# Kernel tuning notes

Measured on AMD Instinct MI355X. Metric: run time of the kernel, lower is better.

Reference implementation:

```python
import jax, jax.numpy as jnp
import numpy as np

N, E, G, C, H, O = 100000, 600000, 1000, 2, 128, 10
HC = H // 2  # cls MLP hidden

def _bn(x, g, b, rm, rv):
    # eval-mode BatchNorm1d with running stats
    return (x - rm) * jax.lax.rsqrt(rv + 1e-5) * g + b

def setup_inputs() -> dict:
    key = jax.random.key(0)
    ks = iter(jax.random.split(key, 64))
    rn = lambda shape, s=0.05: jax.random.normal(next(ks), shape, jnp.float32) * s
    inp = {
        'pos': jax.random.normal(next(ks), (N, C), jnp.float32),
        'edge_index': jax.random.randint(next(ks), (2, E), 0, N),
        'batch': jnp.sort(jax.random.randint(next(ks), (N,), 0, G)),
    }
    def bn_params(pfx):
        return {pfx+'g': jnp.ones((H,), jnp.float32), pfx+'b': jnp.zeros((H,), jnp.float32),
                pfx+'rm': rn((H,)), pfx+'rv': jax.random.uniform(next(ks), (H,), jnp.float32, 0.5, 1.5)}
    # conv1 nn: Lin(C,H)-ReLU-Lin(H,H)-ReLU-BN
    inp.update(W1a=rn((C, H)), b1a=jnp.zeros((H,)), W1b=rn((H, H)), b1b=jnp.zeros((H,)))
    inp.update(bn_params('n1_'))
    # conv2 nn: Lin(H,H)-ReLU-Lin(H,H)-ReLU-BN
    inp.update(W2a=rn((H, H)), b2a=jnp.zeros((H,)), W2b=rn((H, H)), b2b=jnp.zeros((H,)))
    inp.update(bn_params('n2_'))
    # fc1: Lin(C,H)-ReLU-BN ; fc2: Lin(H,H)-ReLU-BN (weights SHARED for both fc2 calls)
    inp.update(Wf1=rn((C, H)), bf1=jnp.zeros((H,)))
    inp.update(bn_params('f1_'))
    inp.update(Wf2=rn((H, H)), bf2=jnp.zeros((H,)))
    inp.update(bn_params('f2_'))
    # cls MLP: Lin(H,HC)-BN-PReLU-Lin(HC,O)
    inp.update(Wc1=rn((H, HC)), bc1=jnp.zeros((HC,)),
               gc=jnp.ones((HC,), jnp.float32), bec=jnp.zeros((HC,), jnp.float32),
               rmc=rn((HC,)), rvc=jax.random.uniform(next(ks), (HC,), jnp.float32, 0.5, 1.5),
               a_prelu=jnp.asarray(0.25, jnp.float32),
               Wc2=rn((HC, O)), bc2=jnp.zeros((O,)))
    return inp


def reference(pos, edge_index, batch,
              W1a, b1a, W1b, b1b, n1_g, n1_b, n1_rm, n1_rv,
              W2a, b2a, W2b, b2b, n2_g, n2_b, n2_rm, n2_rv,
              Wf1, bf1, f1_g, f1_b, f1_rm, f1_rv,
              Wf2, bf2, f2_g, f2_b, f2_rm, f2_rv,
              Wc1, bc1, gc, bec, rmc, rvc, a_prelu, Wc2, bc2):
    src, dst = edge_index[0], edge_index[1]

    def gin_nn(h, Wa, ba, Wb, bb, g, b, rm, rv):
        h = jax.nn.relu(h @ Wa + ba)
        h = jax.nn.relu(h @ Wb + bb)
        return _bn(h, g, b, rm, rv)

    def gin(x, Wa, ba, Wb, bb, g, b, rm, rv):
        # GINConv, eps=0: nn((1+eps)*x + sum_{j in N(i)} x_j)
        agg = jax.ops.segment_sum(x[src], dst, num_segments=N)
        return gin_nn(x + agg, Wa, ba, Wb, bb, g, b, rm, rv)

    def fc(x, W, b, g, be, rm, rv):
        return _bn(jax.nn.relu(x @ W + b), g, be, rm, rv)

    pool = lambda h: jax.ops.segment_sum(h, batch, num_segments=G)

    x0_g = fc(pool(pos), Wf1, bf1, f1_g, f1_b, f1_rm, f1_rv)           # [G,H]
    x1 = gin(pos, W1a, b1a, W1b, b1b, n1_g, n1_b, n1_rm, n1_rv)        # [N,H]
    x1_g = fc(x0_g + pool(x1), Wf2, bf2, f2_g, f2_b, f2_rm, f2_rv)     # [G,H]
    x2 = gin(x1, W2a, b2a, W2b, b2b, n2_g, n2_b, n2_rm, n2_rv)         # [N,H]
    x2_g = fc(x0_g + x1_g + pool(x2), Wf2, bf2, f2_g, f2_b, f2_rm, f2_rv)

    # dropout inactive in eval; cls MLP with PReLU
    h = x2_g @ Wc1 + bc1
    h = _bn(h, gc, bec, rmc, rvc)
    h = jnp.where(h > 0, h, a_prelu * h)
    return h @ Wc2 + bc2  # [G,O]
```

## Files before the change

kernel.cpp:

```cpp
#include <hip/hip_runtime.h>

#define H 128
#define HC 64
#define NOUT 10

static constexpr int kN = 100000;
static constexpr int kE = 600000;
static constexpr int kG = 1000;

typedef __attribute__((ext_vector_type(8))) short short8v;
typedef __attribute__((ext_vector_type(4))) float f32x4;

__device__ __forceinline__ float4 ld4(const float* p) { return *(const float4*)p; }

__device__ __forceinline__ unsigned f2bf(float f) {
    unsigned u = __float_as_uint(f);
    return (u + 0x7fffu + ((u >> 16) & 1u)) >> 16;
}
__device__ __forceinline__ unsigned f2bf2(float a, float b) {
    return f2bf(a) | (f2bf(b) << 16);
}
__device__ __forceinline__ void unpack_add8(uint4 u, float* a) {
    a[0] += __uint_as_float(u.x << 16); a[1] += __uint_as_float(u.x & 0xFFFF0000u);
    a[2] += __uint_as_float(u.y << 16); a[3] += __uint_as_float(u.y & 0xFFFF0000u);
    a[4] += __uint_as_float(u.z << 16); a[5] += __uint_as_float(u.z & 0xFFFF0000u);
    a[6] += __uint_as_float(u.w << 16); a[7] += __uint_as_float(u.w & 0xFFFF0000u);
}

__device__ __forceinline__ int swzmask(int rl) { return (rl & 15) << 3; }

__global__ void k_setup(int* __restrict__ deg,
                        const float* __restrict__ Wa, const float* __restrict__ Wb,
                        const float* __restrict__ Wc, unsigned short* __restrict__ wpk,
                        const int* __restrict__ batch, int* __restrict__ browptr,
                        const float* __restrict__ Wf2, float* __restrict__ Wf2T,
                        const float* __restrict__ Wc1, float* __restrict__ Wc1T) {
    int gt = blockIdx.x * blockDim.x + threadIdx.x;
    if (gt < 25000) {
        ((int4*)deg)[gt] = make_int4(0, 0, 0, 0);
    } else if (gt < 31144) {
        int gt2 = gt - 25000;
        int m = gt2 >> 11, t = gt2 & 2047;
        const float* W = (m == 0) ? Wa : (m == 1) ? Wb : Wc;
        int lane = t & 63, fc = t >> 6;
        int kb = fc >> 3, c16 = fc & 7;
        int col = c16 * 16 + (lane & 15);
        int k0 = kb * 32 + (lane >> 4) * 8;
        unsigned r[4];
#pragma unroll
        for (int p = 0; p < 4; ++p) {
            float a = W[(size_t)(k0 + 2 * p) * H + col];
            float b = W[(size_t)(k0 + 2 * p + 1) * H + col];
            r[p] = f2bf2(a, b);
        }
        *(uint4*)(wpk + (size_t)m * 16384 + (size_t)t * 8) = make_uint4(r[0], r[1], r[2], r[3]);
    } else if (gt < 32145) {
        int g = gt - 31144;
        int lo = 0, hi = kN;
        while (lo < hi) {
            int mid = (lo + hi) >> 1;
            if (batch[mid] < g) lo = mid + 1; else hi = mid;
        }
        browptr[g] = lo;
    } else if (gt < 36241) {
        int id = gt - 32145;
        int col = id >> 5, j4 = id & 31;
        float4 v;
        v.x = Wf2[(j4 * 4 + 0) * H + col];
        v.y = Wf2[(j4 * 4 + 1) * H + col];
        v.z = Wf2[(j4 * 4 + 2) * H + col];
        v.w = Wf2[(j4 * 4 + 3) * H + col];
        ((float4*)Wf2T)[col * 32 + j4] = v;
    } else if (gt < 38289) {
        int id = gt - 36241;
        int t64 = id >> 5, j4 = id & 31;
        float4 v;
        v.x = Wc1[(j4 * 4 + 0) * HC + t64];
        v.y = Wc1[(j4 * 4 + 1) * HC + t64];
        v.z = Wc1[(j4 * 4 + 2) * HC + t64];
        v.w = Wc1[(j4 * 4 + 3) * HC + t64];
        ((float4*)Wc1T)[t64 * 32 + j4] = v;
    }
}

__global__ void k_hist(const int* __restrict__ keys, int* __restrict__ cnt, int n) {
    int i = blockIdx.x * blockDim.x + threadIdx.x;
    if (i < n) atomicAdd(&cnt[keys[i]], 1);
}

__global__ void k_scan_p1(const int* __restrict__ in, int* __restrict__ partial, int n) {
    __shared__ int red[256];
    int b = blockIdx.x, t = threadIdx.x;
    int base = b * 1024 + t * 4;
    int s = 0;
#pragma unroll
    for (int k = 0; k < 4; ++k) {
        int j = base + k;
        if (j < n) s += in[j];
    }
    red[t] = s;
    __syncthreads();
    for (int off = 128; off; off >>= 1) {
        if (t < off) red[t] += red[t + off];
        __syncthreads();
    }
    if (t == 0) partial[b] = red[0];
}

__global__ void k_scan_p3(const int* __restrict__ in, const int* __restrict__ partial,
                          int* __restrict__ out, int* __restrict__ cursor, int n, int nb) {
    __shared__ int bb[256];
    __shared__ int red[256];
    int b = blockIdx.x, t = threadIdx.x;
    bb[t] = (t < b) ? partial[t] : 0;
    __syncthreads();
    for (int off = 128; off; off >>= 1) {
        if (t < off) bb[t] += bb[t + off];
        __syncthreads();
    }
    int bbase = bb[0];

    int base = b * 1024 + t * 4;
    int v[4];
    int s = 0;
#pragma unroll
    for (int k = 0; k < 4; ++k) {
        int j = base + k;
        v[k] = (j < n) ? in[j] : 0;
        s += v[k];
    }
    red[t] = s;
    __syncthreads();
    for (int off = 1; off < 256; off <<= 1) {
        int u = (t >= off) ? red[t - off] : 0;
        __syncthreads();
        red[t] += u;
        __syncthreads();
    }
    int tbase = bbase + red[t] - s;
#pragma unroll
    for (int k = 0; k < 4; ++k) {
        int j = base + k;
        if (j < n) {
            out[j] = tbase;
            if (cursor) cursor[j] = tbase;
            tbase += v[k];
        }
    }
    if (b == nb - 1 && t == 255) out[n] = bbase + red[255];
}

__global__ void k_scatter(const int* __restrict__ src, const int* __restrict__ dst,
                          int* __restrict__ cursor, int* __restrict__ eidx, int E) {
    int e = blockIdx.x * blockDim.x + threadIdx.x;
    if (e >= E) return;
    int slot = atomicAdd(&cursor[dst[e]], 1);
    eidx[slot] = src[e];
}

__global__ void k_gather_add(const int* __restrict__ rowptr, const int* __restrict__ eidx,
                             const unsigned short* __restrict__ x, unsigned short* __restrict__ out,
                             int nN) {
    int idx = blockIdx.x * blockDim.x + threadIdx.x;
    int i = idx >> 4, q = idx & 15;
    if (i >= nN) return;
    const int off = q * 8;
    float a[8] = {0, 0, 0, 0, 0, 0, 0, 0};
    unpack_add8(*(const uint4*)(x + (size_t)i * H + off), a);
    int j0 = rowptr[i], j1 = rowptr[i + 1];
    int j = j0;
    for (; j + 4 <= j1; j += 4) {
        int e0 = eidx[j], e1 = eidx[j + 1], e2 = eidx[j + 2], e3 = eidx[j + 3];
        uint4 u0 = *(const uint4*)(x + (size_t)e0 * H + off);
        uint4 u1 = *(const uint4*)(x + (size_t)e1 * H + off);
        uint4 u2 = *(const uint4*)(x + (size_t)e2 * H + off);
        uint4 u3 = *(const uint4*)(x + (size_t)e3 * H + off);
        unpack_add8(u0, a); unpack_add8(u1, a);
        unpack_add8(u2, a); unpack_add8(u3, a);
    }
    for (; j < j1; ++j) {
        int s = eidx[j];
        unpack_add8(*(const uint4*)(x + (size_t)s * H + off), a);
    }
    *(uint4*)(out + (size_t)i * H + off) =
        make_uint4(f2bf2(a[0], a[1]), f2bf2(a[2], a[3]), f2bf2(a[4], a[5]), f2bf2(a[6], a[7]));
}

__global__ __launch_bounds__(256) void k_gin1(
    const float* __restrict__ pos,
    const int* __restrict__ rowptr, const int* __restrict__ eidx,
    const float* __restrict__ W1a, const float* __restrict__ b1a,
    const short8v* __restrict__ wpk, const float* __restrict__ bias,
    const float* __restrict__ bn_g, const float* __restrict__ bn_b,
    const float* __restrict__ bn_rm, const float* __restrict__ bn_rv,
    unsigned short* __restrict__ out, int nN) {
    __shared__ unsigned short As[H * H];
    __shared__ float sB[H], sS[H], sH2[H];
    const int t = threadIdx.x;

    if (t < H) {
        sB[t] = bias[t];
        float s = bn_g[t] * rsqrtf(bn_rv[t] + 1e-5f);
        sS[t] = s;
        sH2[t] = bn_b[t] - bn_rm[t] * s;
    }

    {
        const int rl = t >> 1, half = t & 1;
        const int ic = min(blockIdx.x * 128 + rl, nN - 1);
        float2 p = ((const float2*)pos)[ic];
        float x0 = half ? 0.f : p.x;
        float x1 = half ? 0.f : p.y;
        int j0 = rowptr[ic], j1 = rowptr[ic + 1];
        int j = j0 + half;
        for (; j + 2 < j1; j += 4) {
            int e0 = eidx[j], e1 = eidx[j + 2];
            float2 q0 = ((const float2*)pos)[e0];
            float2 q1 = ((const float2*)pos)[e1];
            x0 += q0.x + q1.x; x1 += q0.y + q1.y;
        }
        for (; j < j1; j += 2) {
            float2 q = ((const float2*)pos)[eidx[j]];
            x0 += q.x; x1 += q.y;
        }
        x0 += __shfl_xor(x0, 1);
        x1 += __shfl_xor(x1, 1);

        const int mask = swzmask(rl);
#pragma unroll
        for (int c4 = 0; c4 < 16; ++c4) {
            int c = half * 64 + c4 * 4;
            float4 w0 = ld4(&W1a[c]);
            float4 w1 = ld4(&W1a[H + c]);
            float4 bb = ld4(&b1a[c]);
            float r0 = fmaxf(x0 * w0.x + x1 * w1.x + bb.x, 0.f);
            float r1 = fmaxf(x0 * w0.y + x1 * w1.y + bb.y, 0.f);
            float r2 = fmaxf(x0 * w0.z + x1 * w1.z + bb.z, 0.f);
            float r3 = fmaxf(x0 * w0.w + x1 * w1.w + bb.w, 0.f);
            int idx = rl * H + c;
            *(uint2*)(As + (idx ^ mask)) = make_uint2(f2bf2(r0, r1), f2bf2(r2, r3));
        }
    }
    __syncthreads();

    const int lane = t & 63;
    const int wave = t >> 6;
    const int rowbase = blockIdx.x * 128 + wave * 32;
    const int lrow = lane & 15;
    const int lhi = lane >> 4;

    f32x4 acc[2][8];
#pragma unroll
    for (int rr = 0; rr < 2; ++rr)
#pragma unroll
        for (int c = 0; c < 8; ++c) acc[rr][c] = (f32x4){0.f, 0.f, 0.f, 0.f};

#pragma unroll
    for (int kb = 0; kb < 4; ++kb) {
        short8v xf[2];
#pragma unroll
        for (int rr = 0; rr < 2; ++rr) {
            int rl = wave * 32 + rr * 16 + lrow;
            int idx = rl * H + kb * 32 + lhi * 8;
            xf[rr] = *(const short8v*)(As + (idx ^ swzmask(rl)));
        }
#pragma unroll
        for (int c16 = 0; c16 < 8; ++c16) {
            short8v wf = wpk[(kb * 8 + c16) * 64 + lane];
            acc[0][c16] = __builtin_amdgcn_mfma_f32_16x16x32_bf16(wf, xf[0], acc[0][c16], 0, 0, 0);
            acc[1][c16] = __builtin_amdgcn_mfma_f32_16x16x32_bf16(wf, xf[1], acc[1][c16], 0, 0, 0);
        }
    }

#pragma unroll
    for (int c16 = 0; c16 < 8; ++c16) {
        const int c0 = c16 * 16 + lhi * 4;
        float b0 = sB[c0], b1 = sB[c0 + 1], b2 = sB[c0 + 2], b3 = sB[c0 + 3];
        float s0 = sS[c0], s1 = sS[c0 + 1], s2 = sS[c0 + 2], s3 = sS[c0 + 3];
        float h0 = sH2[c0], h1 = sH2[c0 + 1], h2 = sH2[c0 + 2], h3 = sH2[c0 + 3];
#pragma unroll
        for (int rr = 0; rr < 2; ++rr) {
            int row = rowbase + rr * 16 + lrow;
            if (row >= nN) continue;
            float v0 = fmaxf(acc[rr][c16][0] + b0, 0.f) * s0 + h0;
            float v1 = fmaxf(acc[rr][c16][1] + b1, 0.f) * s1 + h1;
            float v2 = fmaxf(acc[rr][c16][2] + b2, 0.f) * s2 + h2;
            float v3 = fmaxf(acc[rr][c16][3] + b3, 0.f) * s3 + h3;
            *(uint2*)(out + (size_t)row * H + c0) = make_uint2(f2bf2(v0, v1), f2bf2(v2, v3));
        }
    }
}

__global__ __launch_bounds__(256) void k_gin2(
    const unsigned short* __restrict__ xin, const short8v* __restrict__ wpA,
    const float* __restrict__ biasA, const short8v* __restrict__ wpB,
    const float* __restrict__ biasB,
    const float* __restrict__ bn_g, const float* __restrict__ bn_b,
    const float* __restrict__ bn_rm, const float* __restrict__ bn_rv,
    unsigned short* __restrict__ out, int nN) {
    __shared__ unsigned short As[H * H];
    __shared__ float sBa[H], sBb[H], sS[H], sH2[H];
    const int t = threadIdx.x;

    if (t < H) {
        sBa[t] = biasA[t];
        sBb[t] = biasB[t];
        float s = bn_g[t] * rsqrtf(bn_rv[t] + 1e-5f);
        sS[t] = s;
        sH2[t] = bn_b[t] - bn_rm[t] * s;
    }
    __syncthreads();

    const int lane = t & 63;
    const int wave = t >> 6;
    const int rowbase = blockIdx.x * 128 + wave * 32;
    const int lrow = lane & 15;
    const int lhi = lane >> 4;

    f32x4 acc[2][8];
#pragma unroll
    for (int rr = 0; rr < 2; ++rr)
#pragma unroll
        for (int c = 0; c < 8; ++c) acc[rr][c] = (f32x4){0.f, 0.f, 0.f, 0.f};

#pragma unroll
    for (int kb = 0; kb < 4; ++kb) {
        short8v xf[2];
#pragma unroll
        for (int rr = 0; rr < 2; ++rr) {
            int row = rowbase + rr * 16 + lrow;
            row = row < nN ? row : nN - 1;
            xf[rr] = *(const short8v*)(xin + (size_t)row * H + kb * 32 + lhi * 8);
        }
#pragma unroll
        for (int c16 = 0; c16 < 8; ++c16) {
            short8v wf = wpA[(kb * 8 + c16) * 64 + lane];
            acc[0][c16] = __builtin_amdgcn_mfma_f32_16x16x32_bf16(wf, xf[0], acc[0][c16], 0, 0, 0);
            acc[1][c16] = __builtin_amdgcn_mfma_f32_16x16x32_bf16(wf, xf[1], acc[1][c16], 0, 0, 0);
        }
    }

#pragma unroll
    for (int c16 = 0; c16 < 8; ++c16) {
        const int c0 = c16 * 16 + lhi * 4;
        float b0 = sBa[c0], b1 = sBa[c0 + 1], b2 = sBa[c0 + 2], b3 = sBa[c0 + 3];
#pragma unroll
        for (int rr = 0; rr < 2; ++rr) {
            int rl = wave * 32 + rr * 16 + lrow;
            float v0 = fmaxf(acc[rr][c16][0] + b0, 0.f);
            float v1 = fmaxf(acc[rr][c16][1] + b1, 0.f);
            float v2 = fmaxf(acc[rr][c16][2] + b2, 0.f);
            float v3 = fmaxf(acc[rr][c16][3] + b3, 0.f);
            int idx = rl * H + c0;
            *(uint2*)(As + (idx ^ swzmask(rl))) = make_uint2(f2bf2(v0, v1), f2bf2(v2, v3));
        }
    }
    __syncthreads();

#pragma unroll
    for (int rr = 0; rr < 2; ++rr)
#pragma unroll
        for (int c = 0; c < 8; ++c) acc[rr][c] = (f32x4){0.f, 0.f, 0.f, 0.f};

#pragma unroll
    for (int kb = 0; kb < 4; ++kb) {
        short8v xf[2];
#pragma unroll
        for (int rr = 0; rr < 2; ++rr) {
            int rl = wave * 32 + rr * 16 + lrow;
            int idx = rl * H + kb * 32 + lhi * 8;
            xf[rr] = *(const short8v*)(As + (idx ^ swzmask(rl)));
        }
#pragma unroll
        for (int c16 = 0; c16 < 8; ++c16) {
            short8v wf = wpB[(kb * 8 + c16) * 64 + lane];
            acc[0][c16] = __builtin_amdgcn_mfma_f32_16x16x32_bf16(wf, xf[0], acc[0][c16], 0, 0, 0);
            acc[1][c16] = __builtin_amdgcn_mfma_f32_16x16x32_bf16(wf, xf[1], acc[1][c16], 0, 0, 0);
        }
    }

#pragma unroll
    for (int c16 = 0; c16 < 8; ++c16) {
        const int c0 = c16 * 16 + lhi * 4;
        float b0 = sBb[c0], b1 = sBb[c0 + 1], b2 = sBb[c0 + 2], b3 = sBb[c0 + 3];
        float s0 = sS[c0], s1 = sS[c0 + 1], s2 = sS[c0 + 2], s3 = sS[c0 + 3];
        float h0 = sH2[c0], h1 = sH2[c0 + 1], h2 = sH2[c0 + 2], h3 = sH2[c0 + 3];
#pragma unroll
        for (int rr = 0; rr < 2; ++rr) {
            int row = rowbase + rr * 16 + lrow;
            if (row >= nN) continue;
            float v0 = fmaxf(acc[rr][c16][0] + b0, 0.f) * s0 + h0;
            float v1 = fmaxf(acc[rr][c16][1] + b1, 0.f) * s1 + h1;
            float v2 = fmaxf(acc[rr][c16][2] + b2, 0.f) * s2 + h2;
            float v3 = fmaxf(acc[rr][c16][3] + b3, 0.f) * s3 + h3;
            *(uint2*)(out + (size_t)row * H + c0) = make_uint2(f2bf2(v0, v1), f2bf2(v2, v3));
        }
    }
}

__global__ __launch_bounds__(256) void k_graph(
    const float* __restrict__ pos,
    const unsigned short* __restrict__ x1, const unsigned short* __restrict__ x2,
    const int* __restrict__ browptr,
    const float* __restrict__ Wf1, const float* __restrict__ bf1,
    const float* __restrict__ f1g, const float* __restrict__ f1b,
    const float* __restrict__ f1rm, const float* __restrict__ f1rv,
    const float* __restrict__ Wf2T, const float* __restrict__ bf2,
    const float* __restrict__ f2g, const float* __restrict__ f2b,
    const float* __restrict__ f2rm, const float* __restrict__ f2rv,
    const float* __restrict__ Wc1T, const float* __restrict__ bc1,
    const float* __restrict__ gc, const float* __restrict__ bec,
    const float* __restrict__ rmc, const float* __restrict__ rvc,
    const float* __restrict__ ap,
    const float* __restrict__ Wc2, const float* __restrict__ bc2,
    float* __restrict__ out) {
    __shared__ float redx[256], redy[256];
    __shared__ float part1[4][16][8], part2[4][16][8];
    __shared__ float row[H];
    __shared__ float hbuf[HC];
    const int gi = blockIdx.x, t = threadIdx.x;
    const int r0 = browptr[gi], r1 = browptr[gi + 1];

    float ax = 0.f, ay = 0.f;
    for (int r = r0 + t; r < r1; r += 256) {
        float2 p = ((const float2*)pos)[r];
        ax += p.x; ay += p.y;
    }
    redx[t] = ax; redy[t] = ay;
    __syncthreads();
    for (int off = 128; off; off >>= 1) {
        if (t < off) { redx[t] += redx[t + off]; redy[t] += redy[t + off]; }
        __syncthreads();
    }
    const float px = redx[0], py = redy[0];

    {
        const int c = t & 15, l = t >> 4;
        float a1[8] = {0, 0, 0, 0, 0, 0, 0, 0};
        float a2[8] = {0, 0, 0, 0, 0, 0, 0, 0};
        for (int r = r0 + l; r < r1; r += 16) {
            unpack_add8(*(const uint4*)(x1 + (size_t)r * H + c * 8), a1);
            unpack_add8(*(const uint4*)(x2 + (size_t)r * H + c * 8), a2);
        }
#pragma unroll
        for (int k = 0; k < 8; ++k) {
            a1[k] += __shfl_xor(a1[k], 16); a1[k] += __shfl_xor(a1[k], 32);
            a2[k] += __shfl_xor(a2[k], 16); a2[k] += __shfl_xor(a2[k], 32);
        }
        const int wv = t >> 6, lane = t & 63;
        if (lane < 16) {
#pragma unroll
            for (int k = 0; k < 8; ++k) {
                part1[wv][lane][k] = a1[k];
                part2[wv][lane][k] = a2[k];
            }
        }
    }
    __syncthreads();

    float x0 = 0.f, p1 = 0.f, p2 = 0.f, s2v = 0.f;
    if (t < H) {
        const int cc = t >> 3, e = t & 7;
        p1 = part1[0][cc][e] + part1[1][cc][e] + part1[2][cc][e] + part1[3][cc][e];
        p2 = part2[0][cc][e] + part2[1][cc][e] + part2[2][cc][e] + part2[3][cc][e];
        float a0 = fmaxf(bf1[t] + px * Wf1[t] + py * Wf1[H + t], 0.f);
        float s1v = f1g[t] * rsqrtf(f1rv[t] + 1e-5f);
        x0 = (a0 - f1rm[t]) * s1v + f1b[t];
        s2v = f2g[t] * rsqrtf(f2rv[t] + 1e-5f);
        row[t] = p1 + x0;
    }
    __syncthreads();

    float x1gv = 0.f;
    if (t < H) {
        float a = bf2[t];
        const float4* wt = (const float4*)(Wf2T + t * H);
#pragma unroll 8
        for (int j4 = 0; j4 < 32; ++j4) {
            float4 w = wt[j4];
            a += row[j4 * 4] * w.x + row[j4 * 4 + 1] * w.y + row[j4 * 4 + 2] * w.z + row[j4 * 4 + 3] * w.w;
        }
        x1gv = (fmaxf(a, 0.f) - f2rm[t]) * s2v + f2b[t];
    }
    __syncthreads();
    if (t < H) row[t] = p2 + x0 + x1gv;
    __syncthreads();

    float x2gv = 0.f;
    if (t < H) {
        float a = bf2[t];
        const float4* wt = (const float4*)(Wf2T + t * H);
#pragma unroll 8
        for (int j4 = 0; j4 < 32; ++j4) {
            float4 w = wt[j4];
            a += row[j4 * 4] * w.x + row[j4 * 4 + 1] * w.y + row[j4 * 4 + 2] * w.z + row[j4 * 4 + 3] * w.w;
        }
        x2gv = (fmaxf(a, 0.f) - f2rm[t]) * s2v + f2b[t];
    }
    __syncthreads();
    if (t < H) row[t] = x2gv;
    __syncthreads();

    if (t < HC) {
        float c = bc1[t];
        const float4* wt = (const float4*)(Wc1T + t * H);
#pragma unroll 8
        for (int j4 = 0; j4 < 32; ++j4) {
            float4 w = wt[j4];
            c += row[j4 * 4] * w.x + row[j4 * 4 + 1] * w.y + row[j4 * 4 + 2] * w.z + row[j4 * 4 + 3] * w.w;
        }
        float sc = gc[t] * rsqrtf(rvc[t] + 1e-5f);
        c = (c - rmc[t]) * sc + bec[t];
        float al = ap[0];
        hbuf[t] = c > 0.f ? c : al * c;
    }
    __syncthreads();
    if (t < NOUT) {
        float c = bc2[t];
        for (int j = 0; j < HC; ++j) c += hbuf[j] * Wc2[j * NOUT + t];
        out[gi * NOUT + t] = c;
    }
}

extern "C" void kernel_launch(void* const* d_in, const int* in_sizes, int n_in,
                              void* d_out, int out_size, void* d_ws, size_t ws_size,
                              hipStream_t stream) {
    const int N = kN, E = kE, G = kG;
    const float* pos = (const float*)d_in[0];
    const int* ei    = (const int*)d_in[1];
    const int* batch = (const int*)d_in[2];
    const float* W1a = (const float*)d_in[3];
    const float* b1a = (const float*)d_in[4];
    const float* W1b = (const float*)d_in[5];
    const float* b1b = (const float*)d_in[6];
    const float* n1g = (const float*)d_in[7];
    const float* n1b = (const float*)d_in[8];
    const float* n1rm = (const float*)d_in[9];
    const float* n1rv = (const float*)d_in[10];
    const float* W2a = (const float*)d_in[11];
    const float* b2a = (const float*)d_in[12];
    const float* W2b = (const float*)d_in[13];
    const float* b2b = (const float*)d_in[14];
    const float* n2g = (const float*)d_in[15];
    const float* n2b = (const float*)d_in[16];
    const float* n2rm = (const float*)d_in[17];
    const float* n2rv = (const float*)d_in[18];
    const float* Wf1 = (const float*)d_in[19];
    const float* bf1 = (const float*)d_in[20];
    const float* f1g = (const float*)d_in[21];
    const float* f1b = (const float*)d_in[22];
    const float* f1rm = (const float*)d_in[23];
    const float* f1rv = (const float*)d_in[24];
    const float* Wf2 = (const float*)d_in[25];
    const float* bf2 = (const float*)d_in[26];
    const float* f2g = (const float*)d_in[27];
    const float* f2b = (const float*)d_in[28];
    const float* f2rm = (const float*)d_in[29];
    const float* f2rv = (const float*)d_in[30];
    const float* Wc1 = (const float*)d_in[31];
    const float* bc1 = (const float*)d_in[32];
    const float* gc  = (const float*)d_in[33];
    const float* bec = (const float*)d_in[34];
    const float* rmc = (const float*)d_in[35];
    const float* rvc = (const float*)d_in[36];
    const float* ap  = (const float*)d_in[37];
    const float* Wc2 = (const float*)d_in[38];
    const float* bc2 = (const float*)d_in[39];
    float* out = (float*)d_out;

    unsigned short* bx1 = (unsigned short*)d_ws;
    unsigned short* bx2 = bx1 + (size_t)N * H;
    unsigned short* wp  = bx2 + (size_t)N * H;
    float* wf2t  = (float*)(wp + 3 * 16384);
    float* wc1t  = wf2t + 16384;
    int* deg     = (int*)(wc1t + 8192);
    int* rowptr  = deg + N;
    int* browptr = rowptr + N + 1;
    int* partial = browptr + G + 1;
    int* eidx    = partial + 1024;

    const short8v* wp1 = (const short8v*)wp;
    const short8v* wp2 = (const short8v*)(wp + 16384);
    const short8v* wp3 = (const short8v*)(wp + 32768);

    const int* src  = ei;
    const int* dstp = ei + E;
    const int nb = (N + 1023) / 1024;

    k_setup<<<150, 256, 0, stream>>>(deg, W1b, W2a, W2b, wp, batch, browptr,
                                     Wf2, wf2t, Wc1, wc1t);
    k_hist<<<(E + 255) / 256, 256, 0, stream>>>(dstp, deg, E);
    k_scan_p1<<<nb, 256, 0, stream>>>(deg, partial, N);
    k_scan_p3<<<nb, 256, 0, stream>>>(deg, partial, rowptr, deg, N, nb);
    k_scatter<<<(E + 255) / 256, 256, 0, stream>>>(src, dstp, deg, eidx, E);

    const int mmBlocks = (N + 127) / 128;

    k_gin1<<<mmBlocks, 256, 0, stream>>>(pos, rowptr, eidx, W1a, b1a, wp1, b1b,
                                         n1g, n1b, n1rm, n1rv, bx1, N);
    k_gather_add<<<(N * 16 + 255) / 256, 256, 0, stream>>>(rowptr, eidx, bx1, bx2, N);
    k_gin2<<<mmBlocks, 256, 0, stream>>>(bx2, wp2, b2a, wp3, b2b,
                                         n2g, n2b, n2rm, n2rv, bx2, N);
    k_graph<<<G, 256, 0, stream>>>(pos, bx1, bx2, browptr,
                                   Wf1, bf1, f1g, f1b, f1rm, f1rv,
                                   wf2t, bf2, f2g, f2b, f2rm, f2rv,
                                   wc1t, bc1, gc, bec, rmc, rvc, ap, Wc2, bc2, out);
}
```

Before: 206.8 us.

## Fuse CSR build and weight setup into one cooperative kernel with grid syncs

```diff
diff --git a/kernel.cpp b/kernel.cpp
--- a/kernel.cpp
+++ b/kernel.cpp
@@ -1,4 +1,7 @@
 #include <hip/hip_runtime.h>
+#include <hip/hip_cooperative_groups.h>
+
+namespace cg = cooperative_groups;
 
 #define H 128
 #define HC 64
@@ -29,20 +32,30 @@
 
 __device__ __forceinline__ int swzmask(int rl) { return (rl & 15) << 3; }
 
-__global__ void k_setup(int* __restrict__ deg,
-                        const float* __restrict__ Wa, const float* __restrict__ Wb,
-                        const float* __restrict__ Wc, unsigned short* __restrict__ wpk,
-                        const int* __restrict__ batch, int* __restrict__ browptr,
-                        const float* __restrict__ Wf2, float* __restrict__ Wf2T,
-                        const float* __restrict__ Wc1, float* __restrict__ Wc1T) {
-    int gt = blockIdx.x * blockDim.x + threadIdx.x;
+__global__ void k_csr(int* __restrict__ deg,
+                      const float* __restrict__ Wa, const float* __restrict__ Wb,
+                      const float* __restrict__ Wc, unsigned short* __restrict__ wpk,
+                      const int* __restrict__ batch, int* __restrict__ browptr,
+                      const float* __restrict__ Wf2, float* __restrict__ Wf2T,
+                      const float* __restrict__ Wc1, float* __restrict__ Wc1T,
+                      const int* __restrict__ src, const int* __restrict__ dstp,
+                      int* __restrict__ rowptr, int* __restrict__ partial,
+                      int* __restrict__ eidx) {
+    cg::grid_group grid = cg::this_grid();
+    const int t = threadIdx.x, bid = blockIdx.x;
+    const int gt = bid * 256 + t;
+    const int GT = 512 * 256;
+
+    __shared__ int red[256];
+    __shared__ int sh[256];
+
     if (gt < 25000) {
         ((int4*)deg)[gt] = make_int4(0, 0, 0, 0);
     } else if (gt < 31144) {
         int gt2 = gt - 25000;
-        int m = gt2 >> 11, t = gt2 & 2047;
+        int m = gt2 >> 11, tt = gt2 & 2047;
         const float* W = (m == 0) ? Wa : (m == 1) ? Wb : Wc;
-        int lane = t & 63, fc = t >> 6;
+        int lane = tt & 63, fc = tt >> 6;
         int kb = fc >> 3, c16 = fc & 7;
         int col = c16 * 16 + (lane & 15);
         int k0 = kb * 32 + (lane >> 4) * 8;
@@ -53,7 +66,7 @@
             float b = W[(size_t)(k0 + 2 * p + 1) * H + col];
             r[p] = f2bf2(a, b);
         }
-        *(uint4*)(wpk + (size_t)m * 16384 + (size_t)t * 8) = make_uint4(r[0], r[1], r[2], r[3]);
+        *(uint4*)(wpk + (size_t)m * 16384 + (size_t)tt * 8) = make_uint4(r[0], r[1], r[2], r[3]);
     } else if (gt < 32145) {
         int g = gt - 31144;
         int lo = 0, hi = kN;
@@ -81,55 +94,32 @@
         v.w = Wc1[(j4 * 4 + 3) * HC + t64];
         ((float4*)Wc1T)[t64 * 32 + j4] = v;
     }
-}
-
-__global__ void k_hist(const int* __restrict__ keys, int* __restrict__ cnt, int n) {
-    int i = blockIdx.x * blockDim.x + threadIdx.x;
-    if (i < n) atomicAdd(&cnt[keys[i]], 1);
-}
-
-__global__ void k_scan_p1(const int* __restrict__ in, int* __restrict__ partial, int n) {
-    __shared__ int red[256];
-    int b = blockIdx.x, t = threadIdx.x;
-    int base = b * 1024 + t * 4;
-    int s = 0;
-#pragma unroll
-    for (int k = 0; k < 4; ++k) {
-        int j = base + k;
-        if (j < n) s += in[j];
-    }
-    red[t] = s;
+    grid.sync();
+
+    for (int e = gt; e < kE; e += GT) atomicAdd(&deg[dstp[e]], 1);
+    grid.sync();
+
+    const int i = gt;
+    int v = (i < kN) ? deg[i] : 0;
+    red[t] = v;
+    sh[t] = v;
     __syncthreads();
     for (int off = 128; off; off >>= 1) {
-        if (t < off) red[t] += red[t + off];
+        if (t < off) sh[t] += sh[t + off];
         __syncthreads();
     }
-    if (t == 0) partial[b] = red[0];
-}
-
-__global__ void k_scan_p3(const int* __restrict__ in, const int* __restrict__ partial,
-                          int* __restrict__ out, int* __restrict__ cursor, int n, int nb) {
-    __shared__ int bb[256];
-    __shared__ int red[256];
-    int b = blockIdx.x, t = threadIdx.x;
-    bb[t] = (t < b) ? partial[t] : 0;
+    if (t == 0) partial[bid] = sh[0];
+    grid.sync();
+
+    int acc0 = ((t < bid) ? partial[t] : 0) + ((t + 256 < bid) ? partial[t + 256] : 0);
+    __syncthreads();
+    sh[t] = acc0;
     __syncthreads();
     for (int off = 128; off; off >>= 1) {
-        if (t < off) bb[t] += bb[t + off];
+        if (t < off) sh[t] += sh[t + off];
         __syncthreads();
     }
-    int bbase = bb[0];
-
-    int base = b * 1024 + t * 4;
-    int v[4];
-    int s = 0;
-#pragma unroll
-    for (int k = 0; k < 4; ++k) {
-        int j = base + k;
-        v[k] = (j < n) ? in[j] : 0;
-        s += v[k];
-    }
-    red[t] = s;
+    const int bbase = sh[0];
     __syncthreads();
     for (int off = 1; off < 256; off <<= 1) {
         int u = (t >= off) ? red[t - off] : 0;
@@ -137,25 +127,16 @@
         red[t] += u;
         __syncthreads();
     }
-    int tbase = bbase + red[t] - s;
-#pragma unroll
-    for (int k = 0; k < 4; ++k) {
-        int j = base + k;
-        if (j < n) {
-            out[j] = tbase;
-            if (cursor) cursor[j] = tbase;
-            tbase += v[k];
-        }
-    }
-    if (b == nb - 1 && t == 255) out[n] = bbase + red[255];
-}
-
-__global__ void k_scatter(const int* __restrict__ src, const int* __restrict__ dst,
-                          int* __restrict__ cursor, int* __restrict__ eidx, int E) {
-    int e = blockIdx.x * blockDim.x + threadIdx.x;
-    if (e >= E) return;
-    int slot = atomicAdd(&cursor[dst[e]], 1);
-    eidx[slot] = src[e];
+    const int incl = red[t];
+    const int tbase = bbase + incl - v;
+    if (i < kN) { rowptr[i] = tbase; deg[i] = tbase; }
+    if (bid == 511 && t == 255) rowptr[kN] = bbase + incl;
+    grid.sync();
+
+    for (int e = gt; e < kE; e += GT) {
+        int slot = atomicAdd(&deg[dstp[e]], 1);
+        eidx[slot] = src[e];
+    }
 }
 
 __global__ void k_gather_add(const int* __restrict__ rowptr, const int* __restrict__ eidx,
@@ -585,14 +566,21 @@
 
     const int* src  = ei;
     const int* dstp = ei + E;
-    const int nb = (N + 1023) / 1024;
-
-    k_setup<<<150, 256, 0, stream>>>(deg, W1b, W2a, W2b, wp, batch, browptr,
-                                     Wf2, wf2t, Wc1, wc1t);
-    k_hist<<<(E + 255) / 256, 256, 0, stream>>>(dstp, deg, E);
-    k_scan_p1<<<nb, 256, 0, stream>>>(deg, partial, N);
-    k_scan_p3<<<nb, 256, 0, stream>>>(deg, partial, rowptr, deg, N, nb);
-    k_scatter<<<(E + 255) / 256, 256, 0, stream>>>(src, dstp, deg, eidx, E);
+
+    {
+        int* a_deg = deg;
+        const float* a_Wa = W1b; const float* a_Wb = W2a; const float* a_Wc = W2b;
+        unsigned short* a_wpk = wp;
+        const int* a_batch = batch; int* a_browptr = browptr;
+        const float* a_Wf2 = Wf2; float* a_wf2t = wf2t;
+        const float* a_Wc1 = Wc1; float* a_wc1t = wc1t;
+        const int* a_src = src; const int* a_dstp = dstp;
+        int* a_rowptr = rowptr; int* a_partial = partial; int* a_eidx = eidx;
+        void* params[] = {&a_deg, &a_Wa, &a_Wb, &a_Wc, &a_wpk, &a_batch, &a_browptr,
+                          &a_Wf2, &a_wf2t, &a_Wc1, &a_wc1t,
+                          &a_src, &a_dstp, &a_rowptr, &a_partial, &a_eidx};
+        hipLaunchCooperativeKernel((void*)k_csr, dim3(512), dim3(256), params, 0, stream);
+    }
 
     const int mmBlocks = (N + 127) / 128;
 
```

Result: slower. 429.1 us (+107.5%).
